# Kernel optimization log

Measured on AMD Instinct MI355X. Metric: run time of the kernel, lower is better.

Reference implementation:

```python
import jax, jax.numpy as jnp
import numpy as np

N_NODES = 100000
N_EDGES = 1000000
F_IN = 64
F_HID = 64
F_OUT = 2
NUM_GRAPHS = 64


def setup_inputs() -> dict:
    key = jax.random.key(0)
    ks = jax.random.split(key, 8)
    x = jax.random.normal(ks[0], (N_NODES, F_IN), dtype=jnp.float32)
    edge_index = jax.random.randint(ks[1], (2, N_EDGES), 0, N_NODES, dtype=jnp.int32)
    batch = jnp.sort(jax.random.randint(ks[2], (N_NODES,), 0, NUM_GRAPHS, dtype=jnp.int32))
    s1 = 1.0 / np.sqrt(F_IN)
    s2 = 1.0 / np.sqrt(F_HID)
    W1 = jax.random.normal(ks[3], (F_IN, F_HID), dtype=jnp.float32) * s1
    W2 = jax.random.normal(ks[4], (F_HID, F_HID), dtype=jnp.float32) * s2
    W3 = jax.random.normal(ks[5], (F_HID, F_HID), dtype=jnp.float32) * s2
    Wlin = jax.random.normal(ks[6], (F_HID, F_OUT), dtype=jnp.float32) * s2
    return {
        "x": x, "edge_index": edge_index, "batch": batch,
        "W1": W1, "b1": jnp.zeros((F_HID,), jnp.float32),
        "W2": W2, "b2": jnp.zeros((F_HID,), jnp.float32),
        "W3": W3, "b3": jnp.zeros((F_HID,), jnp.float32),
        "Wlin": Wlin, "blin": jnp.zeros((F_OUT,), jnp.float32),
    }


def _gcn_norm(edge_index, n_nodes):
    # add self-loops, compute symmetric D^-1/2 (A+I) D^-1/2 edge weights
    loops = jnp.arange(n_nodes, dtype=edge_index.dtype)
    src = jnp.concatenate([edge_index[0], loops])  # message source j
    dst = jnp.concatenate([edge_index[1], loops])  # aggregation target i
    deg = jax.ops.segment_sum(jnp.ones_like(dst, dtype=jnp.float32), dst,
                              num_segments=n_nodes)
    dinv = jnp.where(deg > 0, jax.lax.rsqrt(deg), 0.0)
    norm = dinv[src] * dinv[dst]  # [E+N]
    return src, dst, norm


def _gcn_conv(h, W, b, src, dst, norm, n_nodes):
    h = h @ W                                    # [N, F] dense transform first (PyG order)
    msg = h[src] * norm[:, None]                 # gather + scale  [E+N, F]
    agg = jax.ops.segment_sum(msg, dst, num_segments=n_nodes)
    return agg + b


def reference(x, edge_index, batch, W1, b1, W2, b2, W3, b3, Wlin, blin):
    n = x.shape[0]
    src, dst, norm = _gcn_norm(edge_index, n)
    h = jax.nn.relu(_gcn_conv(x, W1, b1, src, dst, norm, n))
    h = jax.nn.relu(_gcn_conv(h, W2, b2, src, dst, norm, n))
    h = _gcn_conv(h, W3, b3, src, dst, norm, n)
    # global mean pool over graphs
    sums = jax.ops.segment_sum(h, batch, num_segments=NUM_GRAPHS)        # [G, F]
    cnts = jax.ops.segment_sum(jnp.ones((n,), jnp.float32), batch,
                               num_segments=NUM_GRAPHS)
    pooled = sums / jnp.maximum(cnts, 1.0)[:, None]
    # dropout(p=0.1) is identity in eval mode
    return pooled @ Wlin + blin
```

## Files before the change

kernel.cpp:

```cpp
#include <hip/hip_runtime.h>

#define FDIM 64

typedef unsigned short u16;
typedef unsigned int u32;
typedef unsigned long long u64;
typedef float v2f __attribute__((ext_vector_type(2)));

__device__ __forceinline__ u32 pk_fp8x4(float a, float b, float c, float d) {
    u32 p = __builtin_amdgcn_cvt_pk_fp8_f32(a, b, 0, false);
    p = __builtin_amdgcn_cvt_pk_fp8_f32(c, d, p, true);
    return p;
}


template <bool SCALE>
__device__ __forceinline__ void mm_compute(
    u32* __restrict__ t, const int* __restrict__ cnt, int n, int r0,
    float (*__restrict__ As)[FDIM + 1], const float* __restrict__ Ws)
{
    int tid = threadIdx.x;
    int rq = tid >> 4;
    int cq = tid & 15;
    float acc[4][4];
    #pragma unroll
    for (int i = 0; i < 4; ++i)
        #pragma unroll
        for (int j = 0; j < 4; ++j) acc[i][j] = 0.f;

    const float4* Ws4 = (const float4*)Ws;
    #pragma unroll 4
    for (int k = 0; k < FDIM; ++k) {
        float4 w = Ws4[k * 16 + cq];
        float a[4];
        #pragma unroll
        for (int i = 0; i < 4; ++i) a[i] = As[rq * 4 + i][k];
        #pragma unroll
        for (int i = 0; i < 4; ++i) {
            acc[i][0] = fmaf(a[i], w.x, acc[i][0]);
            acc[i][1] = fmaf(a[i], w.y, acc[i][1]);
            acc[i][2] = fmaf(a[i], w.z, acc[i][2]);
            acc[i][3] = fmaf(a[i], w.w, acc[i][3]);
        }
    }

    #pragma unroll
    for (int i = 0; i < 4; ++i) {
        int R = r0 + rq * 4 + i;
        if (R < n) {
            float sc = 1.0f;
            if (SCALE) sc = rsqrtf((float)cnt[R] + 1.0f);
            t[(size_t)R * 16 + cq] =
                pk_fp8x4(acc[i][0] * sc, acc[i][1] * sc,
                         acc[i][2] * sc, acc[i][3] * sc);
        }
    }
}


__global__ __launch_bounds__(256) void k_hist(
    const int* __restrict__ dst, int* __restrict__ hpart,
    u32* __restrict__ zA, u32* __restrict__ zB, int E, int nbuk)
{
    __shared__ int h[1024];
    int tid = threadIdx.x, blk = blockIdx.x;
    if (blk == 0 && tid < 16) { zA[tid] = 0u; zB[tid] = 0u; }
    for (int b = tid; b < nbuk; b += 256) h[b] = 0;
    __syncthreads();
    int stride = gridDim.x * 256;
    for (int e = blk * 256 + tid; e < E; e += stride)
        atomicAdd(&h[dst[e] >> 8], 1);
    __syncthreads();
    for (int b = tid; b < nbuk; b += 256) hpart[b * 256 + blk] = h[b];
}

__global__ __launch_bounds__(256) void k_scan_a(
    int* __restrict__ hpart, int* __restrict__ bb)
{
    __shared__ int s[256];
    int b = blockIdx.x;
    int tid = threadIdx.x;
    int v = hpart[(size_t)b * 256 + tid];
    s[tid] = v;
    __syncthreads();
    #pragma unroll
    for (int off = 1; off < 256; off <<= 1) {
        int w = (tid >= off) ? s[tid - off] : 0;
        __syncthreads();
        s[tid] += w;
        __syncthreads();
    }
    hpart[(size_t)b * 256 + tid] = s[tid] - v;
    if (tid == 255) bb[b] = s[255];
}

__global__ __launch_bounds__(256) void k_scan_b(
    int* __restrict__ bb, int nbuk)
{
    __shared__ int s[512];
    int tid = threadIdx.x;
    s[tid]       = (tid < nbuk) ? bb[tid] : 0;
    s[tid + 256] = (tid + 256 < nbuk) ? bb[tid + 256] : 0;
    __syncthreads();
    #pragma unroll
    for (int off = 1; off < 512; off <<= 1) {
        int a0 = (tid >= off) ? s[tid - off] : 0;
        int a1 = (tid + 256 >= off) ? s[tid + 256 - off] : 0;
        __syncthreads();
        s[tid] += a0;
        s[tid + 256] += a1;
        __syncthreads();
    }
    int e0 = (tid == 0) ? 0 : s[tid - 1];
    int e1 = s[tid + 255];
    if (tid < nbuk) bb[tid] = e0;
    if (tid + 256 < nbuk) bb[tid + 256] = e1;
    if (tid == 255) bb[nbuk] = s[511];
}

__global__ __launch_bounds__(256) void k_scatter(
    const int* __restrict__ src, const int* __restrict__ dst,
    const int* __restrict__ hpart, const int* __restrict__ bb,
    u64* __restrict__ ebuf, int E, int nbuk)
{
    __shared__ int cur[1024];
    int tid = threadIdx.x, blk = blockIdx.x;
    for (int b = tid; b < nbuk; b += 256)
        cur[b] = hpart[(size_t)b * 256 + blk] + bb[b];
    __syncthreads();
    int stride = gridDim.x * 256;
    for (int e = blk * 256 + tid; e < E; e += stride) {
        int d = dst[e], s = src[e];
        int p = atomicAdd(&cur[d >> 8], 1);
        ebuf[p] = ((u64)(u32)d << 32) | (u32)s;
    }
}

__global__ __launch_bounds__(256) void k_build_mm(
    const u64* __restrict__ ebuf, const int* __restrict__ bb,
    int* __restrict__ cnt, int* __restrict__ rptr, int* __restrict__ csr,
    const float* __restrict__ x, const float* __restrict__ W1,
    u32* __restrict__ t, int n, int nbuk)
{
    __shared__ float As[64][FDIM + 1];
    __shared__ float Ws[FDIM * FDIM];
    __shared__ int cnt_l[256], scn[256], cur[256];

    int tid = threadIdx.x;
    if ((int)blockIdx.x < nbuk) {
        int b = blockIdx.x;
        int node0 = b << 8;
        int nn = n - node0; if (nn > 256) nn = 256;
        int e0 = bb[b], e1 = bb[b + 1];

        cnt_l[tid] = 0;
        __syncthreads();
        for (int e = e0 + tid; e < e1; e += 256)
            atomicAdd(&cnt_l[(int)(ebuf[e] >> 32) & 255], 1);
        __syncthreads();
        int v = cnt_l[tid];
        scn[tid] = v;
        __syncthreads();
        #pragma unroll
        for (int off = 1; off < 256; off <<= 1) {
            int w = (tid >= off) ? scn[tid - off] : 0;
            __syncthreads();
            scn[tid] += w;
            __syncthreads();
        }
        int excl = scn[tid] - v;
        if (tid < nn) {
            cnt[node0 + tid]  = v;
            rptr[node0 + tid] = e0 + excl;
        }
        cur[tid] = e0 + excl;
        __syncthreads();
        for (int e = e0 + tid; e < e1; e += 256) {
            u64 pk = ebuf[e];
            int local = (int)(pk >> 32) & 255;
            int p = atomicAdd(&cur[local], 1);
            csr[p] = (int)(u32)(pk & 0xffffffffu);
        }
        return;
    }

    int blk = blockIdx.x - nbuk;
    int r0 = blk * 64;
    #pragma unroll
    for (int i = 0; i < 4; ++i)
        ((float4*)Ws)[tid + 256 * i] = ((const float4*)W1)[tid + 256 * i];
    #pragma unroll
    for (int i = 0; i < 4; ++i) {
        int idx = tid + 256 * i;
        int r = idx >> 4;
        int kq = idx & 15;
        float4 v = make_float4(0.f, 0.f, 0.f, 0.f);
        int R = r0 + r;
        if (R < n) v = ((const float4*)x)[(size_t)R * 16 + kq];
        As[r][kq * 4 + 0] = v.x;
        As[r][kq * 4 + 1] = v.y;
        As[r][kq * 4 + 2] = v.z;
        As[r][kq * 4 + 3] = v.w;
    }
    __syncthreads();
    mm_compute<false>(t, nullptr, n, r0, As, Ws);
}


template <bool SCALED>
__device__ __forceinline__ float4 agg_node(
    int i, const int* __restrict__ cnt, const int* __restrict__ rptr,
    const int* __restrict__ csr, const u32* __restrict__ t,
    int li, int nbase)
{
    int dg = cnt[i];
    float di = rsqrtf((float)dg + 1.0f);
    int m = dg;

    u32 sp = t[(size_t)i * 16 + li];
    v2f s0 = __builtin_amdgcn_cvt_pk_f32_fp8(sp, false);
    v2f s1 = __builtin_amdgcn_cvt_pk_f32_fp8(sp, true);
    float4 A0, A1, A2, A3;
    if (SCALED) {
        A0 = make_float4(s0.x, s0.y, s1.x, s1.y);
    } else {
        A0 = make_float4(s0.x * di, s0.y * di, s1.x * di, s1.y * di);
    }
    A1 = make_float4(0.f, 0.f, 0.f, 0.f);
    A2 = make_float4(0.f, 0.f, 0.f, 0.f);
    A3 = make_float4(0.f, 0.f, 0.f, 0.f);

    const int* row = csr + rptr[i];

    for (int c0 = 0; c0 < m; c0 += 16) {
        int cm = m - c0; if (cm > 16) cm = 16;
        int sv = -1; float dvv = 0.f;
        if (li < cm) {
            sv = __builtin_nontemporal_load(&row[c0 + li]);
            if (!SCALED) dvv = rsqrtf((float)cnt[sv] + 1.0f);
        }
        int jv[16]; float dj[16]; u32 v[16];
        #pragma unroll
        for (int u = 0; u < 16; ++u) {
            jv[u] = __shfl(sv, nbase + u);
            if (!SCALED) dj[u] = __shfl(dvv, nbase + u);
        }
        #pragma unroll
        for (int u = 0; u < 16; ++u)
            v[u] = t[(long long)jv[u] * 16 + li];
        #pragma unroll
        for (int u = 0; u < 16; ++u) {
            v2f x0 = __builtin_amdgcn_cvt_pk_f32_fp8(v[u], false);
            v2f x1 = __builtin_amdgcn_cvt_pk_f32_fp8(v[u], true);
            float4* Ap = (u & 3) == 0 ? &A0 : (u & 3) == 1 ? &A1 :
                         (u & 3) == 2 ? &A2 : &A3;
            if (SCALED) {
                Ap->x += x0.x; Ap->y += x0.y;
                Ap->z += x1.x; Ap->w += x1.y;
            } else {
                Ap->x = fmaf(x0.x, dj[u], Ap->x);
                Ap->y = fmaf(x0.y, dj[u], Ap->y);
                Ap->z = fmaf(x1.x, dj[u], Ap->z);
                Ap->w = fmaf(x1.y, dj[u], Ap->w);
            }
        }
    }

    float4 O;
    O.x = ((A0.x + A1.x) + (A2.x + A3.x)) * di;
    O.y = ((A0.y + A1.y) + (A2.y + A3.y)) * di;
    O.z = ((A0.z + A1.z) + (A2.z + A3.z)) * di;
    O.w = ((A0.w + A1.w) + (A2.w + A3.w)) * di;
    return O;
}


template <bool SCALED_IN>
__global__ __launch_bounds__(256) void k_aggmm(
    const int* __restrict__ cnt, const int* __restrict__ rptr,
    const int* __restrict__ csr, const u32* __restrict__ tin,
    const float* __restrict__ Wm, const float* __restrict__ bias,
    u32* __restrict__ tout, int n)
{
    __shared__ float As[64][FDIM + 1];
    __shared__ float Ws[FDIM * FDIM];
    int tid = threadIdx.x;
    #pragma unroll
    for (int i = 0; i < 4; ++i)
        ((float4*)Ws)[tid + 256 * i] = ((const float4*)Wm)[tid + 256 * i];

    int r0 = blockIdx.x * 64;
    int group = tid >> 4;
    int li = tid & 15;
    int nbase = ((tid & 63) >> 4) << 4;
    float4 b = ((const float4*)bias)[li];

    #pragma unroll 1
    for (int r = 0; r < 4; ++r) {
        int row = r * 16 + group;
        int i = r0 + row;
        float4 v = make_float4(0.f, 0.f, 0.f, 0.f);
        if (i < n) {
            float4 O = agg_node<SCALED_IN>(i, cnt, rptr, csr, tin, li, nbase);
            v.x = fmaxf(O.x + b.x, 0.f);
            v.y = fmaxf(O.y + b.y, 0.f);
            v.z = fmaxf(O.z + b.z, 0.f);
            v.w = fmaxf(O.w + b.w, 0.f);
        }
        As[row][li * 4 + 0] = v.x;
        As[row][li * 4 + 1] = v.y;
        As[row][li * 4 + 2] = v.z;
        As[row][li * 4 + 3] = v.w;
    }
    __syncthreads();
    mm_compute<true>(tout, cnt, n, r0, As, Ws);
}


__global__ __launch_bounds__(256) void k_agg_pool(
    const int* __restrict__ cnt, const int* __restrict__ rptr,
    const int* __restrict__ csr, const u32* __restrict__ t,
    const int* __restrict__ batch, float* __restrict__ partial,
    int n, int npart)
{
    int g = blockIdx.x / npart;
    int part = blockIdx.x - g * npart;
    int tid = threadIdx.x;

    int lo = 0, hi = n;
    while (lo < hi) { int mid = (lo + hi) >> 1; if (batch[mid] < g) lo = mid + 1; else hi = mid; }
    int start = lo;
    hi = n;
    while (lo < hi) { int mid = (lo + hi) >> 1; if (batch[mid] <= g) lo = mid + 1; else hi = mid; }
    int end = lo;

    int group = tid >> 4;
    int li = tid & 15;
    int nbase = ((tid & 63) >> 4) << 4;

    float4 acc = make_float4(0.f, 0.f, 0.f, 0.f);
    for (int i = start + part * 16 + group; i < end; i += npart * 16) {
        float4 O = agg_node<true>(i, cnt, rptr, csr, t, li, nbase);
        acc.x += O.x; acc.y += O.y; acc.z += O.z; acc.w += O.w;
    }

    __shared__ float4 red[16][16];
    red[group][li] = acc;
    __syncthreads();
    if (tid < 16) {
        float4 s = make_float4(0.f, 0.f, 0.f, 0.f);
        #pragma unroll
        for (int q = 0; q < 16; ++q) {
            s.x += red[q][tid].x; s.y += red[q][tid].y;
            s.z += red[q][tid].z; s.w += red[q][tid].w;
        }
        ((float4*)partial)[((size_t)g * npart + part) * 16 + tid] = s;
    }
}


__global__ __launch_bounds__(64) void k_pool2(
    const float* __restrict__ partial, const int* __restrict__ batch,
    const float* __restrict__ b3, const float* __restrict__ Wlin,
    const float* __restrict__ blin, float* __restrict__ out,
    int n, int fout, int npart)
{
    int g = blockIdx.x;
    int tid = threadIdx.x;

    int lo = 0, hi = n;
    while (lo < hi) { int mid = (lo + hi) >> 1; if (batch[mid] < g) lo = mid + 1; else hi = mid; }
    int start = lo;
    hi = n;
    while (lo < hi) { int mid = (lo + hi) >> 1; if (batch[mid] <= g) lo = mid + 1; else hi = mid; }
    int cg = lo - start;

    __shared__ float pooled[64];
    float v = 0.f;
    for (int p = 0; p < npart; ++p)
        v += partial[((size_t)g * npart + p) * 64 + tid];
    pooled[tid] = (cg > 0) ? (v / (float)cg + b3[tid]) : 0.f;
    __syncthreads();
    if (tid < fout) {
        float o = blin[tid];
        for (int k = 0; k < 64; ++k) o += pooled[k] * Wlin[k * fout + tid];
        out[(size_t)g * fout + tid] = o;
    }
}


extern "C" void kernel_launch(void* const* d_in, const int* in_sizes, int n_in,
                              void* d_out, int out_size, void* d_ws, size_t ws_size,
                              hipStream_t stream) {
    const float* x     = (const float*)d_in[0];
    const int*   ei    = (const int*)d_in[1];
    const int*   batch = (const int*)d_in[2];
    const float* W1 = (const float*)d_in[3];
    const float* b1 = (const float*)d_in[4];
    const float* W2 = (const float*)d_in[5];
    const float* b2 = (const float*)d_in[6];
    const float* W3 = (const float*)d_in[7];
    const float* b3 = (const float*)d_in[8];
    const float* Wl = (const float*)d_in[9];
    const float* bl = (const float*)d_in[10];

    int n = in_sizes[0] / 64;
    int E = in_sizes[1] / 2;
    int fout = in_sizes[10];
    int ngraphs = out_size / fout;

    const int* srcp = ei;
    const int* dstp = ei + E;

    const int npart = 16;
    int nbuk = (n + 255) >> 8;

    u64* ebuf = (u64*)d_ws;
    int* csr  = (int*)(ebuf + (size_t)E);
    int* cnt  = csr + (size_t)E;
    int* rptr = cnt + n;
    int* bb   = rptr + n;
    int* hpart = bb + (nbuk + 1);
    u32* zA  = (u32*)(hpart + (size_t)nbuk * 256);
    u32* tA  = zA + 16;
    u32* zB  = tA + (size_t)n * 16;
    u32* tB  = zB + 16;
    float* ppool = (float*)(tB + (size_t)n * 16);

    int mm_blocks = (n + 63) / 64;

    k_hist<<<256, 256, 0, stream>>>(dstp, hpart, zA, zB, E, nbuk);
    k_scan_a<<<nbuk, 256, 0, stream>>>(hpart, bb);
    k_scan_b<<<1, 256, 0, stream>>>(bb, nbuk);
    k_scatter<<<256, 256, 0, stream>>>(srcp, dstp, hpart, bb, ebuf, E, nbuk);
    k_build_mm<<<nbuk + mm_blocks, 256, 0, stream>>>(
        ebuf, bb, cnt, rptr, csr, x, W1, tA, n, nbuk);

    k_aggmm<false><<<mm_blocks, 256, 0, stream>>>(cnt, rptr, csr, tA, W2, b1, tB, n);
    k_aggmm<true><<<mm_blocks, 256, 0, stream>>>(cnt, rptr, csr, tB, W3, b2, tA, n);
    k_agg_pool<<<ngraphs * npart, 256, 0, stream>>>(
        cnt, rptr, csr, tA, batch, ppool, n, npart);
    k_pool2<<<ngraphs, 64, 0, stream>>>(ppool, batch, b3, Wl, bl,
                                        (float*)d_out, n, fout, npart);
}
```

Measured before the change: 245.4 us.

## Co-schedule first-layer matmul with histogram and stage aggregated rows as bf16

The layer-1 dense transform (x@W1) moves out of the CSR build kernel and into the histogram kernel, so the matmul blocks run alongside the edge histogram rather than behind the scan and scatter steps. CSR build becomes a standalone kernel. In the fused aggregate+matmul kernels, the post-ReLU activation tile is stored in LDS as packed bf16 instead of fp32, halving LDS footprint, which may raise occupancy. The cost is extra unpack work per FMA and reduced precision of the intermediate activations.

```diff
diff --git a/kernel.cpp b/kernel.cpp
--- a/kernel.cpp
+++ b/kernel.cpp
@@ -7,6 +7,13 @@
 typedef unsigned long long u64;
 typedef float v2f __attribute__((ext_vector_type(2)));
 
+__device__ __forceinline__ u16 f2bf(float x) {
+    unsigned int u = __float_as_uint(x);
+    return (u16)((u + 0x7fff + ((u >> 16) & 1)) >> 16);
+}
+__device__ __forceinline__ float bf2f(u16 h) {
+    return __uint_as_float(((unsigned int)h) << 16);
+}
 __device__ __forceinline__ u32 pk_fp8x4(float a, float b, float c, float d) {
     u32 p = __builtin_amdgcn_cvt_pk_fp8_f32(a, b, 0, false);
     p = __builtin_amdgcn_cvt_pk_fp8_f32(c, d, p, true);
@@ -58,134 +65,81 @@
 }
 
 
-__global__ __launch_bounds__(256) void k_hist(
+__device__ __forceinline__ void mm_compute_bf16(
+    u32* __restrict__ t, const int* __restrict__ cnt, int n, int r0,
+    u32 (*__restrict__ Asb)[33], const float* __restrict__ Ws)
+{
+    int tid = threadIdx.x;
+    int rq = tid >> 4;
+    int cq = tid & 15;
+    float acc[4][4];
+    #pragma unroll
+    for (int i = 0; i < 4; ++i)
+        #pragma unroll
+        for (int j = 0; j < 4; ++j) acc[i][j] = 0.f;
+
+    const float4* Ws4 = (const float4*)Ws;
+    #pragma unroll 4
+    for (int k2 = 0; k2 < FDIM / 2; ++k2) {
+        float4 w0 = Ws4[(2 * k2) * 16 + cq];
+        float4 w1 = Ws4[(2 * k2 + 1) * 16 + cq];
+        float a0[4], a1[4];
+        #pragma unroll
+        for (int i = 0; i < 4; ++i) {
+            u32 pk = Asb[rq * 4 + i][k2];
+            a0[i] = bf2f((u16)(pk & 0xffff));
+            a1[i] = bf2f((u16)(pk >> 16));
+        }
+        #pragma unroll
+        for (int i = 0; i < 4; ++i) {
+            acc[i][0] = fmaf(a0[i], w0.x, acc[i][0]);
+            acc[i][1] = fmaf(a0[i], w0.y, acc[i][1]);
+            acc[i][2] = fmaf(a0[i], w0.z, acc[i][2]);
+            acc[i][3] = fmaf(a0[i], w0.w, acc[i][3]);
+            acc[i][0] = fmaf(a1[i], w1.x, acc[i][0]);
+            acc[i][1] = fmaf(a1[i], w1.y, acc[i][1]);
+            acc[i][2] = fmaf(a1[i], w1.z, acc[i][2]);
+            acc[i][3] = fmaf(a1[i], w1.w, acc[i][3]);
+        }
+    }
+
+    #pragma unroll
+    for (int i = 0; i < 4; ++i) {
+        int R = r0 + rq * 4 + i;
+        if (R < n) {
+            float sc = rsqrtf((float)cnt[R] + 1.0f);
+            t[(size_t)R * 16 + cq] =
+                pk_fp8x4(acc[i][0] * sc, acc[i][1] * sc,
+                         acc[i][2] * sc, acc[i][3] * sc);
+        }
+    }
+}
+
+
+__global__ __launch_bounds__(256) void k_hist_mm(
     const int* __restrict__ dst, int* __restrict__ hpart,
-    u32* __restrict__ zA, u32* __restrict__ zB, int E, int nbuk)
-{
-    __shared__ int h[1024];
-    int tid = threadIdx.x, blk = blockIdx.x;
-    if (blk == 0 && tid < 16) { zA[tid] = 0u; zB[tid] = 0u; }
-    for (int b = tid; b < nbuk; b += 256) h[b] = 0;
-    __syncthreads();
-    int stride = gridDim.x * 256;
-    for (int e = blk * 256 + tid; e < E; e += stride)
-        atomicAdd(&h[dst[e] >> 8], 1);
-    __syncthreads();
-    for (int b = tid; b < nbuk; b += 256) hpart[b * 256 + blk] = h[b];
-}
-
-__global__ __launch_bounds__(256) void k_scan_a(
-    int* __restrict__ hpart, int* __restrict__ bb)
-{
-    __shared__ int s[256];
-    int b = blockIdx.x;
-    int tid = threadIdx.x;
-    int v = hpart[(size_t)b * 256 + tid];
-    s[tid] = v;
-    __syncthreads();
-    #pragma unroll
-    for (int off = 1; off < 256; off <<= 1) {
-        int w = (tid >= off) ? s[tid - off] : 0;
-        __syncthreads();
-        s[tid] += w;
-        __syncthreads();
-    }
-    hpart[(size_t)b * 256 + tid] = s[tid] - v;
-    if (tid == 255) bb[b] = s[255];
-}
-
-__global__ __launch_bounds__(256) void k_scan_b(
-    int* __restrict__ bb, int nbuk)
-{
-    __shared__ int s[512];
-    int tid = threadIdx.x;
-    s[tid]       = (tid < nbuk) ? bb[tid] : 0;
-    s[tid + 256] = (tid + 256 < nbuk) ? bb[tid + 256] : 0;
-    __syncthreads();
-    #pragma unroll
-    for (int off = 1; off < 512; off <<= 1) {
-        int a0 = (tid >= off) ? s[tid - off] : 0;
-        int a1 = (tid + 256 >= off) ? s[tid + 256 - off] : 0;
-        __syncthreads();
-        s[tid] += a0;
-        s[tid + 256] += a1;
-        __syncthreads();
-    }
-    int e0 = (tid == 0) ? 0 : s[tid - 1];
-    int e1 = s[tid + 255];
-    if (tid < nbuk) bb[tid] = e0;
-    if (tid + 256 < nbuk) bb[tid + 256] = e1;
-    if (tid == 255) bb[nbuk] = s[511];
-}
-
-__global__ __launch_bounds__(256) void k_scatter(
-    const int* __restrict__ src, const int* __restrict__ dst,
-    const int* __restrict__ hpart, const int* __restrict__ bb,
-    u64* __restrict__ ebuf, int E, int nbuk)
-{
-    __shared__ int cur[1024];
-    int tid = threadIdx.x, blk = blockIdx.x;
-    for (int b = tid; b < nbuk; b += 256)
-        cur[b] = hpart[(size_t)b * 256 + blk] + bb[b];
-    __syncthreads();
-    int stride = gridDim.x * 256;
-    for (int e = blk * 256 + tid; e < E; e += stride) {
-        int d = dst[e], s = src[e];
-        int p = atomicAdd(&cur[d >> 8], 1);
-        ebuf[p] = ((u64)(u32)d << 32) | (u32)s;
-    }
-}
-
-__global__ __launch_bounds__(256) void k_build_mm(
-    const u64* __restrict__ ebuf, const int* __restrict__ bb,
-    int* __restrict__ cnt, int* __restrict__ rptr, int* __restrict__ csr,
+    u32* __restrict__ zA, u32* __restrict__ zB,
     const float* __restrict__ x, const float* __restrict__ W1,
-    u32* __restrict__ t, int n, int nbuk)
+    u32* __restrict__ t, int n, int E, int nbuk, int hist_blocks)
 {
     __shared__ float As[64][FDIM + 1];
     __shared__ float Ws[FDIM * FDIM];
-    __shared__ int cnt_l[256], scn[256], cur[256];
-
-    int tid = threadIdx.x;
-    if ((int)blockIdx.x < nbuk) {
-        int b = blockIdx.x;
-        int node0 = b << 8;
-        int nn = n - node0; if (nn > 256) nn = 256;
-        int e0 = bb[b], e1 = bb[b + 1];
-
-        cnt_l[tid] = 0;
-        __syncthreads();
-        for (int e = e0 + tid; e < e1; e += 256)
-            atomicAdd(&cnt_l[(int)(ebuf[e] >> 32) & 255], 1);
-        __syncthreads();
-        int v = cnt_l[tid];
-        scn[tid] = v;
-        __syncthreads();
-        #pragma unroll
-        for (int off = 1; off < 256; off <<= 1) {
-            int w = (tid >= off) ? scn[tid - off] : 0;
-            __syncthreads();
-            scn[tid] += w;
-            __syncthreads();
-        }
-        int excl = scn[tid] - v;
-        if (tid < nn) {
-            cnt[node0 + tid]  = v;
-            rptr[node0 + tid] = e0 + excl;
-        }
-        cur[tid] = e0 + excl;
-        __syncthreads();
-        for (int e = e0 + tid; e < e1; e += 256) {
-            u64 pk = ebuf[e];
-            int local = (int)(pk >> 32) & 255;
-            int p = atomicAdd(&cur[local], 1);
-            csr[p] = (int)(u32)(pk & 0xffffffffu);
-        }
+    __shared__ int h[1024];
+
+    int tid = threadIdx.x, blk = blockIdx.x;
+    if ((int)blk < hist_blocks) {
+        if (blk == 0 && tid < 16) { zA[tid] = 0u; zB[tid] = 0u; }
+        for (int b = tid; b < nbuk; b += 256) h[b] = 0;
+        __syncthreads();
+        int stride = hist_blocks * 256;
+        for (int e = blk * 256 + tid; e < E; e += stride)
+            atomicAdd(&h[dst[e] >> 8], 1);
+        __syncthreads();
+        for (int b = tid; b < nbuk; b += 256) hpart[b * 256 + blk] = h[b];
         return;
     }
 
-    int blk = blockIdx.x - nbuk;
-    int r0 = blk * 64;
+    int r0 = (blk - hist_blocks) * 64;
     #pragma unroll
     for (int i = 0; i < 4; ++i)
         ((float4*)Ws)[tid + 256 * i] = ((const float4*)W1)[tid + 256 * i];
@@ -204,6 +158,110 @@
     }
     __syncthreads();
     mm_compute<false>(t, nullptr, n, r0, As, Ws);
+}
+
+__global__ __launch_bounds__(256) void k_scan_a(
+    int* __restrict__ hpart, int* __restrict__ bb)
+{
+    __shared__ int s[256];
+    int b = blockIdx.x;
+    int tid = threadIdx.x;
+    int v = hpart[(size_t)b * 256 + tid];
+    s[tid] = v;
+    __syncthreads();
+    #pragma unroll
+    for (int off = 1; off < 256; off <<= 1) {
+        int w = (tid >= off) ? s[tid - off] : 0;
+        __syncthreads();
+        s[tid] += w;
+        __syncthreads();
+    }
+    hpart[(size_t)b * 256 + tid] = s[tid] - v;
+    if (tid == 255) bb[b] = s[255];
+}
+
+__global__ __launch_bounds__(256) void k_scan_b(
+    int* __restrict__ bb, int nbuk)
+{
+    __shared__ int s[512];
+    int tid = threadIdx.x;
+    s[tid]       = (tid < nbuk) ? bb[tid] : 0;
+    s[tid + 256] = (tid + 256 < nbuk) ? bb[tid + 256] : 0;
+    __syncthreads();
+    #pragma unroll
+    for (int off = 1; off < 512; off <<= 1) {
+        int a0 = (tid >= off) ? s[tid - off] : 0;
+        int a1 = (tid + 256 >= off) ? s[tid + 256 - off] : 0;
+        __syncthreads();
+        s[tid] += a0;
+        s[tid + 256] += a1;
+        __syncthreads();
+    }
+    int e0 = (tid == 0) ? 0 : s[tid - 1];
+    int e1 = s[tid + 255];
+    if (tid < nbuk) bb[tid] = e0;
+    if (tid + 256 < nbuk) bb[tid + 256] = e1;
+    if (tid == 255) bb[nbuk] = s[511];
+}
+
+__global__ __launch_bounds__(256) void k_scatter(
+    const int* __restrict__ src, const int* __restrict__ dst,
+    const int* __restrict__ hpart, const int* __restrict__ bb,
+    u64* __restrict__ ebuf, int E, int nbuk)
+{
+    __shared__ int cur[1024];
+    int tid = threadIdx.x, blk = blockIdx.x;
+    for (int b = tid; b < nbuk; b += 256)
+        cur[b] = hpart[(size_t)b * 256 + blk] + bb[b];
+    __syncthreads();
+    int stride = gridDim.x * 256;
+    for (int e = blk * 256 + tid; e < E; e += stride) {
+        int d = dst[e], s = src[e];
+        int p = atomicAdd(&cur[d >> 8], 1);
+        ebuf[p] = ((u64)(u32)d << 32) | (u32)s;
+    }
+}
+
+__global__ __launch_bounds__(256) void k_build(
+    const u64* __restrict__ ebuf, const int* __restrict__ bb,
+    int* __restrict__ cnt, int* __restrict__ rptr, int* __restrict__ csr,
+    int n)
+{
+    __shared__ int cnt_l[256], scn[256], cur[256];
+    int tid = threadIdx.x;
+    int b = blockIdx.x;
+    int node0 = b << 8;
+    int nn = n - node0; if (nn > 256) nn = 256;
+    int e0 = bb[b], e1 = bb[b + 1];
+
+    cnt_l[tid] = 0;
+    __syncthreads();
+    for (int e = e0 + tid; e < e1; e += 256)
+        atomicAdd(&cnt_l[(int)(ebuf[e] >> 32) & 255], 1);
+    __syncthreads();
+    int v = cnt_l[tid];
+    scn[tid] = v;
+    __syncthreads();
+    #pragma unroll
+    for (int off = 1; off < 256; off <<= 1) {
+        int w = (tid >= off) ? scn[tid - off] : 0;
+        __syncthreads();
+        scn[tid] += w;
+        __syncthreads();
+    }
+    int excl = scn[tid] - v;
+    if (tid < nn) {
+        cnt[node0 + tid]  = v;
+        rptr[node0 + tid] = e0 + excl;
+    }
+    cur[tid] = e0 + excl;
+    __syncthreads();
+    for (int e = e0 + tid; e < e1; e += 256) {
+        u64 pk = ebuf[e];
+        int local = (int)(pk >> 32) & 255;
+        int p = atomicAdd(&cur[local], 1);
+        csr[p] = (int)(u32)(pk & 0xffffffffu);
+    }
 }
 
 
@@ -282,7 +340,7 @@
     const float* __restrict__ Wm, const float* __restrict__ bias,
     u32* __restrict__ tout, int n)
 {
-    __shared__ float As[64][FDIM + 1];
+    __shared__ u32 Asb[64][33];
     __shared__ float Ws[FDIM * FDIM];
     int tid = threadIdx.x;
     #pragma unroll
@@ -307,13 +365,11 @@
             v.z = fmaxf(O.z + b.z, 0.f);
             v.w = fmaxf(O.w + b.w, 0.f);
         }
-        As[row][li * 4 + 0] = v.x;
-        As[row][li * 4 + 1] = v.y;
-        As[row][li * 4 + 2] = v.z;
-        As[row][li * 4 + 3] = v.w;
-    }
-    __syncthreads();
-    mm_compute<true>(tout, cnt, n, r0, As, Ws);
+        Asb[row][li * 2 + 0] = ((u32)f2bf(v.x)) | (((u32)f2bf(v.y)) << 16);
+        Asb[row][li * 2 + 1] = ((u32)f2bf(v.z)) | (((u32)f2bf(v.w)) << 16);
+    }
+    __syncthreads();
+    mm_compute_bf16(tout, cnt, n, r0, Asb, Ws);
 }
 
 
@@ -428,13 +484,14 @@
     float* ppool = (float*)(tB + (size_t)n * 16);
 
     int mm_blocks = (n + 63) / 64;
-
-    k_hist<<<256, 256, 0, stream>>>(dstp, hpart, zA, zB, E, nbuk);
+    int hist_blocks = 256;
+
+    k_hist_mm<<<hist_blocks + mm_blocks, 256, 0, stream>>>(
+        dstp, hpart, zA, zB, x, W1, tA, n, E, nbuk, hist_blocks);
     k_scan_a<<<nbuk, 256, 0, stream>>>(hpart, bb);
     k_scan_b<<<1, 256, 0, stream>>>(bb, nbuk);
     k_scatter<<<256, 256, 0, stream>>>(srcp, dstp, hpart, bb, ebuf, E, nbuk);
-    k_build_mm<<<nbuk + mm_blocks, 256, 0, stream>>>(
-        ebuf, bb, cnt, rptr, csr, x, W1, tA, n, nbuk);
+    k_build<<<nbuk, 256, 0, stream>>>(ebuf, bb, cnt, rptr, csr, n);
 
     k_aggmm<false><<<mm_blocks, 256, 0, stream>>>(cnt, rptr, csr, tA, W2, b1, tB, n);
     k_aggmm<true><<<mm_blocks, 256, 0, stream>>>(cnt, rptr, csr, tB, W3, b2, tA, n);
```

Result: no change. 244.3 us, median of 2 (-0.4%).
